# Optimization experiments

Measured on AMD Instinct MI355X. Metric: run time of the kernel, lower is better.

## Reference

```python
import jax, jax.numpy as jnp
import numpy as np
from functools import partial

IN_CH, OUT_CH, HID = 16, 20, 256
B, T = 64, 4096
LEAKY_SLOPE = 0.01  # torch LeakyReLU default


def _lstm_layer(x_seq, Wih, Whh, bih, bhh):
    """Single-layer LSTM over a full sequence.

    x_seq: (T, B, Din). Weights use PyTorch layout: W (4H, Din/H), gate order i,f,g,o.
    Returns hidden states (T, B, H).
    """
    H = Whh.shape[1]
    Tlen, Bsz = x_seq.shape[0], x_seq.shape[1]
    # Precompute input contributions for all timesteps in one GEMM.
    xw = jnp.einsum('tbd,gd->tbg', x_seq, Wih) + (bih + bhh)  # (T, B, 4H)

    def step(carry, xw_t):
        h, c = carry
        gates = xw_t + h @ Whh.T  # (B, 4H)
        i, f, g, o = jnp.split(gates, 4, axis=-1)
        i = jax.nn.sigmoid(i)
        f = jax.nn.sigmoid(f)
        g = jnp.tanh(g)
        o = jax.nn.sigmoid(o)
        c = f * c + i * g
        h = o * jnp.tanh(c)
        return (h, c), h

    h0 = jnp.zeros((Bsz, H), dtype=x_seq.dtype)
    c0 = jnp.zeros((Bsz, H), dtype=x_seq.dtype)
    _, hs = jax.lax.scan(step, (h0, c0), xw)
    return hs  # (T, B, H)


def setup_inputs() -> dict:
    key = jax.random.key(0)
    ks = jax.random.split(key, 12)
    s = 1.0 / np.sqrt(HID)  # torch nn.LSTM init scale
    return {
        'x': jax.random.normal(ks[0], (B, IN_CH, T), dtype=jnp.float32),
        'Wih0': jax.random.normal(ks[1], (4 * HID, IN_CH), dtype=jnp.float32) * s,
        'Whh0': jax.random.normal(ks[2], (4 * HID, HID), dtype=jnp.float32) * s,
        'bih0': jax.random.normal(ks[3], (4 * HID,), dtype=jnp.float32) * s,
        'bhh0': jax.random.normal(ks[4], (4 * HID,), dtype=jnp.float32) * s,
        'Wih1': jax.random.normal(ks[5], (4 * HID, HID), dtype=jnp.float32) * s,
        'Whh1': jax.random.normal(ks[6], (4 * HID, HID), dtype=jnp.float32) * s,
        'bih1': jax.random.normal(ks[7], (4 * HID,), dtype=jnp.float32) * s,
        'bhh1': jax.random.normal(ks[8], (4 * HID,), dtype=jnp.float32) * s,
        'Whead': jax.random.normal(ks[9], (OUT_CH, HID), dtype=jnp.float32) * s,
        'bhead': jax.random.normal(ks[10], (OUT_CH,), dtype=jnp.float32) * s,
    }


def reference(x, Wih0, Whh0, bih0, bhh0, Wih1, Whh1, bih1, bhh1, Whead, bhead):
    # x: (B, C_in, T) -> time-major (T, B, C_in)
    xs = jnp.transpose(x, (2, 0, 1))
    h1 = _lstm_layer(xs, Wih0, Whh0, bih0, bhh0)   # (T, B, H)
    h2 = _lstm_layer(h1, Wih1, Whh1, bih1, bhh1)   # (T, B, H)
    # Head: LeakyReLU then Linear, applied per timestep (vectorized).
    a = jnp.where(h2 >= 0, h2, LEAKY_SLOPE * h2)
    y = jnp.einsum('tbh,oh->tbo', a, Whead) + bhead  # (T, B, OUT)
    return jnp.transpose(y, (1, 2, 0))  # (B, C_out, T)
```

## Files before the change

### kernel.cpp

```cpp
#include <hip/hip_runtime.h>
#include <hip/hip_fp16.h>
#include <stdint.h>


#define T_SEQ 4096
#define NB    64
#define HID   256
#define G4    1024
#define INCH  16
#define OC    20

typedef _Float16 h2v   __attribute__((ext_vector_type(2)));
typedef _Float16 f16x8 __attribute__((ext_vector_type(8)));
typedef float    f32x4 __attribute__((ext_vector_type(4)));

__device__ __forceinline__ float fdot2(uint32_t a, uint32_t b, float c) {
  return __builtin_amdgcn_fdot2(__builtin_bit_cast(h2v, a),
                                __builtin_bit_cast(h2v, b), c, false);
}
__device__ __forceinline__ float sigf(float x) {
  x = fminf(fmaxf(x, -30.f), 30.f);
  return 1.f / (1.f + __expf(-x));
}
__device__ __forceinline__ float tanhf_fast(float x) {
  x = fminf(fmaxf(x, -15.f), 15.f);
  float e = __expf(-2.f * x);
  return (1.f - e) / (1.f + e);
}
__device__ __forceinline__ float quad_sum(float a) {
  a += __int_as_float(
      __builtin_amdgcn_update_dpp(0, __float_as_int(a), 0xB1, 0xF, 0xF, true));
  a += __int_as_float(
      __builtin_amdgcn_update_dpp(0, __float_as_int(a), 0x4E, 0xF, 0xF, true));
  return a;
}

#define PIN(x) asm volatile("" : "+v"(x))

struct SmemR {
  __half w[256 * 264];
  uint32_t hbuf[2][144];
  union {
    uint32_t xb[512 * 8];
    struct {
      __half abuf[2][320];
      __half whd[20 * 264];
      float  bh[20];
    } h1;
  } u;
};
struct SmemG {
  __half a[128 * 40];
  __half b[64 * 40];
};
union Smem { SmemR r; SmemG g; };

struct Params {
  const float* x;
  const __half *wh0, *wh1, *wi0, *wi1, *whd;
  const float  *bs0, *bs1, *bhd;
  float *h0s, *c0s, *h1s, *c1s;
  __half* h1w; const __half* h1r;
  float* xww;  const float* xwr;
  float* y;
  int L, Tc, nch;
};

template <int LAYER>
__device__ void role_rec(SmemR& S, int ch, const Params& P, int b) {
  if (ch < 0 || ch >= P.nch) return;
  const int tid   = threadIdx.x;
  const int slice = tid & 3;
  const int rg    = tid >> 2;
  const int Tc    = P.Tc;
  const __half* whh = (LAYER == 0) ? P.wh0 : P.wh1;

  for (int i = tid; i < 8192; i += 512) {
    int R = i >> 5, oct = i & 31;
    *(uint4*)&S.w[R * 264 + oct * 8] =
        *((const uint4*)(whh + (768 + R) * 256) + oct);
  }
  const int t0 = ch * Tc;
  if (LAYER == 0) {
    for (int i = tid; i < Tc * 8; i += 512) {
      int dp = i / Tc, tt = i - dp * Tc;
      float v0 = P.x[(b * INCH + 2 * dp) * T_SEQ + t0 + tt];
      float v1 = P.x[(b * INCH + 2 * dp + 1) * T_SEQ + t0 + tt];
      uint32_t pv = (uint32_t)__half_as_ushort(__float2half(v0)) |
                    ((uint32_t)__half_as_ushort(__float2half(v1)) << 16);
      S.u.xb[tt * 8 + dp] = pv;
    }
  } else {
    for (int i = tid; i < OC * 256; i += 512) {
      int o = i >> 8, k = i & 255;
      S.u.h1.whd[o * 264 + k] = P.whd[i];
    }
    if (tid < OC) S.u.h1.bh[tid] = P.bhd[tid];
  }

  uint32_t wr[6][32];
#pragma unroll
  for (int j = 0; j < 6; j++) {
    const uint4* p = (const uint4*)(whh + (rg + 128 * j) * 256 + slice * 64);
#pragma unroll
    for (int q = 0; q < 8; q++) {
      uint4 v = p[q];
      wr[j][4 * q] = v.x; wr[j][4 * q + 1] = v.y;
      wr[j][4 * q + 2] = v.z; wr[j][4 * q + 3] = v.w;
    }
  }
#pragma unroll
  for (int j = 0; j < 6; j++)
#pragma unroll
    for (int q = 0; q < 32; q++) PIN(wr[j][q]);

  uint32_t wx[8][2];
  if (LAYER == 0) {
#pragma unroll
    for (int j = 0; j < 8; j++) {
      const uint32_t* p = (const uint32_t*)(P.wi0 + (rg + 128 * j) * INCH + slice * 4);
      wx[j][0] = p[0]; wx[j][1] = p[1];
    }
#pragma unroll
    for (int j = 0; j < 8; j++) { PIN(wx[j][0]); PIN(wx[j][1]); }
  }

  const bool own = (slice < 2);
  const int chn = rg + ((slice & 1) << 7);
  float* hs = (LAYER == 0) ? P.h0s : P.h1s;
  float* cs = (LAYER == 0) ? P.c0s : P.c1s;
  float bs4[4] = {0.f, 0.f, 0.f, 0.f};
  float hO = 0.f, cO = 0.f;
  if (own) {
    const float* bsg = (LAYER == 0) ? P.bs0 : P.bs1;
#pragma unroll
    for (int k = 0; k < 4; k++) bs4[k] = bsg[chn + 256 * k];
    if (ch != 0) { hO = hs[b * 256 + chn]; cO = cs[b * 256 + chn]; }
    ((__half*)S.hbuf[0])[(chn >> 6) * 72 + (chn & 63)] = __float2half(hO);
  }
  const float* xp = (LAYER == 1 && own) ? (P.xwr + (size_t)b * G4 + chn)
                                        : (const float*)nullptr;
  __syncthreads();

  const __half* hbA = (const __half*)S.hbuf[0] + slice * 72;
  const __half* hbB = (const __half*)S.hbuf[1] + slice * 72;
  __half hprev = __float2half(0.f);
  float xwv[4] = {0.f, 0.f, 0.f, 0.f};

  for (int tt = 0; tt < Tc; ++tt) {
    if (LAYER == 0 && own && tt > 0)
      P.h1w[(size_t)((tt - 1) * NB + b) * 256 + chn] = hprev;
    if (LAYER == 1 && own) {
      const float* q = xp + (size_t)tt * (NB * G4);
      xwv[0] = q[0]; xwv[1] = q[256]; xwv[2] = q[512]; xwv[3] = q[768];
    }

    const __half* hb = (tt & 1) ? hbB : hbA;
    float acc[8];
#pragma unroll
    for (int j = 0; j < 8; j++) acc[j] = 0.f;

#pragma unroll
    for (int hf = 0; hf < 2; ++hf) {
      uint32_t hh[16];
      const uint4* hp = (const uint4*)(hb + hf * 32);
#pragma unroll
      for (int q = 0; q < 4; q++) {
        uint4 v = hp[q];
        hh[4 * q] = v.x; hh[4 * q + 1] = v.y; hh[4 * q + 2] = v.z; hh[4 * q + 3] = v.w;
      }
#pragma unroll
      for (int j = 0; j < 6; j++) {
        float a = acc[j];
#pragma unroll
        for (int q = 0; q < 16; q++) a = fdot2(wr[j][hf * 16 + q], hh[q], a);
        acc[j] = a;
      }
#pragma unroll
      for (int j = 6; j < 8; j++) {
        const uint4* wp =
            (const uint4*)&S.w[((j - 6) * 128 + rg) * 264 + slice * 64 + hf * 32];
        float a = acc[j];
#pragma unroll
        for (int q = 0; q < 4; q++) {
          uint4 v = wp[q];
          a = fdot2(v.x, hh[4 * q], a);
          a = fdot2(v.y, hh[4 * q + 1], a);
          a = fdot2(v.z, hh[4 * q + 2], a);
          a = fdot2(v.w, hh[4 * q + 3], a);
        }
        acc[j] = a;
      }
    }
    if (LAYER == 0) {
      uint32_t xv0 = S.u.xb[tt * 8 + 2 * slice];
      uint32_t xv1 = S.u.xb[tt * 8 + 2 * slice + 1];
#pragma unroll
      for (int j = 0; j < 8; j++) {
        acc[j] = fdot2(wx[j][0], xv0, acc[j]);
        acc[j] = fdot2(wx[j][1], xv1, acc[j]);
      }
    }
#pragma unroll
    for (int j = 0; j < 8; j++) acc[j] = quad_sum(acc[j]);

    if (own) {
      const int o = slice & 1;
      float gi = acc[0 + o] + bs4[0];
      float gf = acc[2 + o] + bs4[1];
      float gg = acc[4 + o] + bs4[2];
      float go = acc[6 + o] + bs4[3];
      if (LAYER == 1) { gi += xwv[0]; gf += xwv[1]; gg += xwv[2]; go += xwv[3]; }
      float iv = sigf(gi), fv = sigf(gf);
      float gv = tanhf_fast(gg), ov = sigf(go);
      cO = fv * cO + iv * gv;
      hO = ov * tanhf_fast(cO);
      __half h16 = __float2half(hO);
      ((__half*)S.hbuf[(tt + 1) & 1])[(chn >> 6) * 72 + (chn & 63)] = h16;
      if (LAYER == 0) {
        hprev = h16;
      } else {
        float av = hO > 0.f ? hO : 0.01f * hO;
        S.u.h1.abuf[tt & 1][(chn >> 5) * 40 + (chn & 31)] = __float2half(av);
      }
    }
    __syncthreads();

    if (LAYER == 1 && tid < OC * 8) {
      int o = tid >> 3, ks = tid & 7;
      const uint4* wp = (const uint4*)&S.u.h1.whd[o * 264 + ks * 32];
      const uint4* ap = (const uint4*)&S.u.h1.abuf[tt & 1][ks * 40];
      float a = 0.f;
#pragma unroll
      for (int q = 0; q < 4; q++) {
        uint4 w4 = wp[q];
        uint4 a4 = ap[q];
        a = fdot2(w4.x, a4.x, a);
        a = fdot2(w4.y, a4.y, a);
        a = fdot2(w4.z, a4.z, a);
        a = fdot2(w4.w, a4.w, a);
      }
      a += __shfl_xor(a, 1);
      a += __shfl_xor(a, 2);
      a += __shfl_xor(a, 4);
      if (ks == 0) P.y[(b * OC + o) * T_SEQ + t0 + tt] = a + S.u.h1.bh[o];
    }
  }
  if (own) {
    if (LAYER == 0)
      P.h1w[(size_t)((Tc - 1) * NB + b) * 256 + chn] = hprev;
    hs[b * 256 + chn] = hO;
    cs[b * 256 + chn] = cO;
  }
}

__device__ void role_gemm(SmemG& S, int chG, const Params& P) {
  if (chG < 0 || chG >= P.nch) return;
  const int bid = blockIdx.x - 128;
  const int nt = bid & 15, mt = bid >> 4;
  const int tb0 = mt * 128, g0 = nt * 64;
  const int tid = threadIdx.x, lane = tid & 63, w = tid >> 6;
  const int wm = w & 3, wn = w >> 2;

  f32x4 cacc[2][2] = {};
  for (int kk = 0; kk < 256; kk += 32) {
    __syncthreads();
    {
      int row = tid >> 2, q = tid & 3;
      const uint4* src = (const uint4*)(P.h1r + (tb0 + row) * 256 + kk + q * 8);
      *(uint4*)&S.a[row * 40 + q * 8] = *src;
    }
    if (tid < 256) {
      int row = tid >> 2, q = tid & 3;
      const uint4* src = (const uint4*)(P.wi1 + (g0 + row) * 256 + kk + q * 8);
      *(uint4*)&S.b[row * 40 + q * 8] = *src;
    }
    __syncthreads();
    f16x8 af[2], bf[2];
#pragma unroll
    for (int mi = 0; mi < 2; mi++)
      af[mi] = *(const f16x8*)&S.a[(wm * 32 + mi * 16 + (lane & 15)) * 40 + (lane >> 4) * 8];
#pragma unroll
    for (int ni = 0; ni < 2; ni++)
      bf[ni] = *(const f16x8*)&S.b[(wn * 32 + ni * 16 + (lane & 15)) * 40 + (lane >> 4) * 8];
#pragma unroll
    for (int mi = 0; mi < 2; mi++)
#pragma unroll
      for (int ni = 0; ni < 2; ni++)
        cacc[mi][ni] = __builtin_amdgcn_mfma_f32_16x16x32_f16(af[mi], bf[ni], cacc[mi][ni], 0, 0, 0);
  }
#pragma unroll
  for (int mi = 0; mi < 2; mi++)
#pragma unroll
    for (int ni = 0; ni < 2; ni++) {
      int m = wm * 32 + mi * 16 + (lane >> 4) * 4;
      int n = g0 + wn * 32 + ni * 16 + (lane & 15);
#pragma unroll
      for (int r = 0; r < 4; r++)
        P.xww[(size_t)(tb0 + m + r) * G4 + n] = cacc[mi][ni][r];
    }
}

__global__ __launch_bounds__(512)
__attribute__((amdgpu_waves_per_eu(2, 2)))
void fused_kernel(Params P) {
  __shared__ Smem S;
  int bid = blockIdx.x;
  if (bid < 64)        role_rec<0>(S.r, P.L, P, bid);
  else if (bid < 128)  role_rec<1>(S.r, P.L - 2, P, bid - 64);
  else                 role_gemm(S.g, P.L - 1, P);
}

__global__ void prep_kernel(const float* Wih0, const float* Whh0,
                            const float* bih0, const float* bhh0,
                            const float* Wih1, const float* Whh1,
                            const float* bih1, const float* bhh1,
                            const float* Whead, const float* bhead,
                            __half* wh0, __half* wh1, __half* wi1, __half* wi0,
                            __half* whd, float* bs0, float* bs1, float* bhd) {
  int i = blockIdx.x * blockDim.x + threadIdx.x;
  if (i < G4 * HID) {
    wh0[i] = __float2half(Whh0[i]);
    wh1[i] = __float2half(Whh1[i]);
    wi1[i] = __float2half(Wih1[i]);
  }
  if (i < G4 * INCH) wi0[i] = __float2half(Wih0[i]);
  if (i < OC * HID)  whd[i] = __float2half(Whead[i]);
  if (i < G4) { bs0[i] = bih0[i] + bhh0[i]; bs1[i] = bih1[i] + bhh1[i]; }
  if (i < OC) bhd[i] = bhead[i];
}

extern "C" void kernel_launch(void* const* d_in, const int* in_sizes, int n_in,
                              void* d_out, int out_size, void* d_ws, size_t ws_size,
                              hipStream_t stream) {
  const float* x     = (const float*)d_in[0];
  const float* Wih0  = (const float*)d_in[1];
  const float* Whh0  = (const float*)d_in[2];
  const float* bih0  = (const float*)d_in[3];
  const float* bhh0  = (const float*)d_in[4];
  const float* Wih1  = (const float*)d_in[5];
  const float* Whh1  = (const float*)d_in[6];
  const float* bih1  = (const float*)d_in[7];
  const float* bhh1  = (const float*)d_in[8];
  const float* Whead = (const float*)d_in[9];
  const float* bhead = (const float*)d_in[10];
  float* y = (float*)d_out;

  char* ws = (char*)d_ws;
  size_t cur = 0;
  auto alloc = [&](size_t sz) -> char* {
    char* p = ws + cur;
    cur = (cur + sz + 255) & ~(size_t)255;
    return p;
  };
  __half* wh0 = (__half*)alloc(G4 * HID * 2);
  __half* wh1 = (__half*)alloc(G4 * HID * 2);
  __half* wi1 = (__half*)alloc(G4 * HID * 2);
  __half* wi0 = (__half*)alloc(G4 * INCH * 2);
  __half* whd = (__half*)alloc(OC * HID * 2);
  float* bs0 = (float*)alloc(G4 * 4);
  float* bs1 = (float*)alloc(G4 * 4);
  float* bhd = (float*)alloc(OC * 4);
  float* h0s = (float*)alloc(NB * HID * 4);
  float* c0s = (float*)alloc(NB * HID * 4);
  float* h1s = (float*)alloc(NB * HID * 4);
  float* c1s = (float*)alloc(NB * HID * 4);
  size_t fixed = cur;

  int Tc = 512;
  while (Tc > 64) {
    size_t need = fixed + 2 * ((size_t)Tc * NB * HID * 2 + 512) +
                  2 * ((size_t)Tc * NB * G4 * 4 + 512);
    if (need <= ws_size) break;
    Tc >>= 1;
  }
  __half* h1buf[2];
  float* xwbuf[2];
  h1buf[0] = (__half*)alloc((size_t)Tc * NB * HID * 2);
  h1buf[1] = (__half*)alloc((size_t)Tc * NB * HID * 2);
  xwbuf[0] = (float*)alloc((size_t)Tc * NB * G4 * 4);
  xwbuf[1] = (float*)alloc((size_t)Tc * NB * G4 * 4);

  const int nch = T_SEQ / Tc;

  prep_kernel<<<(G4 * HID + 255) / 256, 256, 0, stream>>>(
      Wih0, Whh0, bih0, bhh0, Wih1, Whh1, bih1, bhh1, Whead, bhead,
      wh0, wh1, wi1, wi0, whd, bs0, bs1, bhd);

  const int ngemm = Tc * 8;
  for (int L = 0; L < nch + 2; ++L) {
    Params P;
    P.x = x;
    P.wh0 = wh0; P.wh1 = wh1; P.wi0 = wi0; P.wi1 = wi1; P.whd = whd;
    P.bs0 = bs0; P.bs1 = bs1; P.bhd = bhd;
    P.h0s = h0s; P.c0s = c0s; P.h1s = h1s; P.c1s = c1s;
    P.h1w = h1buf[L & 1];
    P.h1r = h1buf[(L + 1) & 1];
    P.xww = xwbuf[(L + 1) & 1];
    P.xwr = xwbuf[L & 1];
    P.y = y;
    P.L = L; P.Tc = Tc; P.nch = nch;
    fused_kernel<<<128 + ngemm, 512, 0, stream>>>(P);
  }
}
```

Measured before the change: 9.867 ms.

## Precompute layer-0 input projection one chunk ahead and store xw buffers in fp16

```diff
diff --git a/kernel.cpp b/kernel.cpp
--- a/kernel.cpp
+++ b/kernel.cpp
@@ -61,10 +61,54 @@
   const float  *bs0, *bs1, *bhd;
   float *h0s, *c0s, *h1s, *c1s;
   __half* h1w; const __half* h1r;
-  float* xww;  const float* xwr;
+  __half* xw1w; const __half* xw1r;
+  __half* xw0w; const __half* xw0r;
   float* y;
   int L, Tc, nch;
 };
+
+__device__ void compute_xw0(SmemR& S, int cc, const Params& P, int b,
+                            __half* out) {
+  const int tid = threadIdx.x;
+  const int Tc  = P.Tc;
+  const int t0  = cc * Tc;
+  for (int i = tid; i < Tc * 8; i += 512) {
+    int dp = i / Tc, tt = i - dp * Tc;
+    float v0 = P.x[(b * INCH + 2 * dp) * T_SEQ + t0 + tt];
+    float v1 = P.x[(b * INCH + 2 * dp + 1) * T_SEQ + t0 + tt];
+    uint32_t pv = (uint32_t)__half_as_ushort(__float2half(v0)) |
+                  ((uint32_t)__half_as_ushort(__float2half(v1)) << 16);
+    S.u.xb[tt * 8 + dp] = pv;
+  }
+  __syncthreads();
+  uint32_t w0[8], w1[8];
+  {
+    const uint4* p0 = (const uint4*)(P.wi0 + tid * INCH);
+    const uint4* p1 = (const uint4*)(P.wi0 + (tid + 512) * INCH);
+    uint4 a0 = p0[0], a1 = p0[1], b0 = p1[0], b1 = p1[1];
+    w0[0] = a0.x; w0[1] = a0.y; w0[2] = a0.z; w0[3] = a0.w;
+    w0[4] = a1.x; w0[5] = a1.y; w0[6] = a1.z; w0[7] = a1.w;
+    w1[0] = b0.x; w1[1] = b0.y; w1[2] = b0.z; w1[3] = b0.w;
+    w1[4] = b1.x; w1[5] = b1.y; w1[6] = b1.z; w1[7] = b1.w;
+  }
+  for (int tt = 0; tt < Tc; ++tt) {
+    uint32_t xv[8];
+    const uint4* xp = (const uint4*)&S.u.xb[tt * 8];
+    uint4 v0 = xp[0], v1 = xp[1];
+    xv[0] = v0.x; xv[1] = v0.y; xv[2] = v0.z; xv[3] = v0.w;
+    xv[4] = v1.x; xv[5] = v1.y; xv[6] = v1.z; xv[7] = v1.w;
+    float a0 = 0.f, a1 = 0.f;
+#pragma unroll
+    for (int q = 0; q < 8; ++q) {
+      a0 = fdot2(w0[q], xv[q], a0);
+      a1 = fdot2(w1[q], xv[q], a1);
+    }
+    __half* o = out + (size_t)(tt * NB + b) * G4;
+    o[tid]       = __float2half(a0);
+    o[tid + 512] = __float2half(a1);
+  }
+  __syncthreads();
+}
 
 template <int LAYER>
 __device__ void role_rec(SmemR& S, int ch, const Params& P, int b) {
@@ -82,14 +126,8 @@
   }
   const int t0 = ch * Tc;
   if (LAYER == 0) {
-    for (int i = tid; i < Tc * 8; i += 512) {
-      int dp = i / Tc, tt = i - dp * Tc;
-      float v0 = P.x[(b * INCH + 2 * dp) * T_SEQ + t0 + tt];
-      float v1 = P.x[(b * INCH + 2 * dp + 1) * T_SEQ + t0 + tt];
-      uint32_t pv = (uint32_t)__half_as_ushort(__float2half(v0)) |
-                    ((uint32_t)__half_as_ushort(__float2half(v1)) << 16);
-      S.u.xb[tt * 8 + dp] = pv;
-    }
+    if (ch == 0) compute_xw0(S, 0, P, b, P.xw0w == nullptr ? nullptr : (__half*)P.xw0r);
+    if (ch + 1 < P.nch) compute_xw0(S, ch + 1, P, b, P.xw0w);
   } else {
     for (int i = tid; i < OC * 256; i += 512) {
       int o = i >> 8, k = i & 255;
@@ -113,17 +151,6 @@
   for (int j = 0; j < 6; j++)
 #pragma unroll
     for (int q = 0; q < 32; q++) PIN(wr[j][q]);
-
-  uint32_t wx[8][2];
-  if (LAYER == 0) {
-#pragma unroll
-    for (int j = 0; j < 8; j++) {
-      const uint32_t* p = (const uint32_t*)(P.wi0 + (rg + 128 * j) * INCH + slice * 4);
-      wx[j][0] = p[0]; wx[j][1] = p[1];
-    }
-#pragma unroll
-    for (int j = 0; j < 8; j++) { PIN(wx[j][0]); PIN(wx[j][1]); }
-  }
 
   const bool own = (slice < 2);
   const int chn = rg + ((slice & 1) << 7);
@@ -138,67 +165,68 @@
     if (ch != 0) { hO = hs[b * 256 + chn]; cO = cs[b * 256 + chn]; }
     ((__half*)S.hbuf[0])[(chn >> 6) * 72 + (chn & 63)] = __float2half(hO);
   }
-  const float* xp = (LAYER == 1 && own) ? (P.xwr + (size_t)b * G4 + chn)
-                                        : (const float*)nullptr;
+  const __half* xp = nullptr;
+  if (own) xp = ((LAYER == 0) ? P.xw0r : P.xw1r) + (size_t)b * G4 + chn;
   __syncthreads();
 
   const __half* hbA = (const __half*)S.hbuf[0] + slice * 72;
   const __half* hbB = (const __half*)S.hbuf[1] + slice * 72;
+  const __half* wbase6 = &S.w[rg * 264 + slice * 64];
+  const __half* wbase7 = &S.w[(128 + rg) * 264 + slice * 64];
   __half hprev = __float2half(0.f);
-  float xwv[4] = {0.f, 0.f, 0.f, 0.f};
 
   for (int tt = 0; tt < Tc; ++tt) {
     if (LAYER == 0 && own && tt > 0)
       P.h1w[(size_t)((tt - 1) * NB + b) * 256 + chn] = hprev;
-    if (LAYER == 1 && own) {
-      const float* q = xp + (size_t)tt * (NB * G4);
-      xwv[0] = q[0]; xwv[1] = q[256]; xwv[2] = q[512]; xwv[3] = q[768];
+    float xwv[4] = {0.f, 0.f, 0.f, 0.f};
+    if (own) {
+      const __half* q = xp + (size_t)tt * (NB * G4);
+      xwv[0] = __half2float(q[0]);
+      xwv[1] = __half2float(q[256]);
+      xwv[2] = __half2float(q[512]);
+      xwv[3] = __half2float(q[768]);
     }
 
     const __half* hb = (tt & 1) ? hbB : hbA;
+    const uint4* hp = (const uint4*)hb;
     float acc[8];
 #pragma unroll
     for (int j = 0; j < 8; j++) acc[j] = 0.f;
 
 #pragma unroll
-    for (int hf = 0; hf < 2; ++hf) {
-      uint32_t hh[16];
-      const uint4* hp = (const uint4*)(hb + hf * 32);
-#pragma unroll
-      for (int q = 0; q < 4; q++) {
-        uint4 v = hp[q];
-        hh[4 * q] = v.x; hh[4 * q + 1] = v.y; hh[4 * q + 2] = v.z; hh[4 * q + 3] = v.w;
-      }
-#pragma unroll
-      for (int j = 0; j < 6; j++) {
+    for (int sb = 0; sb < 4; ++sb) {
+      uint32_t hh[8];
+      {
+        uint4 v0 = hp[2 * sb], v1 = hp[2 * sb + 1];
+        hh[0] = v0.x; hh[1] = v0.y; hh[2] = v0.z; hh[3] = v0.w;
+        hh[4] = v1.x; hh[5] = v1.y; hh[6] = v1.z; hh[7] = v1.w;
+      }
+#pragma unroll
+      for (int j = 0; j < 6; ++j) {
         float a = acc[j];
 #pragma unroll
-        for (int q = 0; q < 16; q++) a = fdot2(wr[j][hf * 16 + q], hh[q], a);
+        for (int q = 0; q < 8; ++q) a = fdot2(wr[j][8 * sb + q], hh[q], a);
         acc[j] = a;
       }
-#pragma unroll
-      for (int j = 6; j < 8; j++) {
-        const uint4* wp =
-            (const uint4*)&S.w[((j - 6) * 128 + rg) * 264 + slice * 64 + hf * 32];
-        float a = acc[j];
-#pragma unroll
-        for (int q = 0; q < 4; q++) {
-          uint4 v = wp[q];
-          a = fdot2(v.x, hh[4 * q], a);
-          a = fdot2(v.y, hh[4 * q + 1], a);
-          a = fdot2(v.z, hh[4 * q + 2], a);
-          a = fdot2(v.w, hh[4 * q + 3], a);
-        }
-        acc[j] = a;
-      }
-    }
-    if (LAYER == 0) {
-      uint32_t xv0 = S.u.xb[tt * 8 + 2 * slice];
-      uint32_t xv1 = S.u.xb[tt * 8 + 2 * slice + 1];
-#pragma unroll
-      for (int j = 0; j < 8; j++) {
-        acc[j] = fdot2(wx[j][0], xv0, acc[j]);
-        acc[j] = fdot2(wx[j][1], xv1, acc[j]);
+      {
+        const uint4* wp = (const uint4*)(wbase6 + sb * 16);
+        uint4 w0 = wp[0], w1 = wp[1];
+        float a = acc[6];
+        a = fdot2(w0.x, hh[0], a); a = fdot2(w0.y, hh[1], a);
+        a = fdot2(w0.z, hh[2], a); a = fdot2(w0.w, hh[3], a);
+        a = fdot2(w1.x, hh[4], a); a = fdot2(w1.y, hh[5], a);
+        a = fdot2(w1.z, hh[6], a); a = fdot2(w1.w, hh[7], a);
+        acc[6] = a;
+      }
+      {
+        const uint4* wp = (const uint4*)(wbase7 + sb * 16);
+        uint4 w0 = wp[0], w1 = wp[1];
+        float a = acc[7];
+        a = fdot2(w0.x, hh[0], a); a = fdot2(w0.y, hh[1], a);
+        a = fdot2(w0.z, hh[2], a); a = fdot2(w0.w, hh[3], a);
+        a = fdot2(w1.x, hh[4], a); a = fdot2(w1.y, hh[5], a);
+        a = fdot2(w1.z, hh[6], a); a = fdot2(w1.w, hh[7], a);
+        acc[7] = a;
       }
     }
 #pragma unroll
@@ -206,11 +234,10 @@
 
     if (own) {
       const int o = slice & 1;
-      float gi = acc[0 + o] + bs4[0];
-      float gf = acc[2 + o] + bs4[1];
-      float gg = acc[4 + o] + bs4[2];
-      float go = acc[6 + o] + bs4[3];
-      if (LAYER == 1) { gi += xwv[0]; gf += xwv[1]; gg += xwv[2]; go += xwv[3]; }
+      float gi = acc[0 + o] + bs4[0] + xwv[0];
+      float gf = acc[2 + o] + bs4[1] + xwv[1];
+      float gg = acc[4 + o] + bs4[2] + xwv[2];
+      float go = acc[6 + o] + bs4[3] + xwv[3];
       float iv = sigf(gi), fv = sigf(gf);
       float gv = tanhf_fast(gg), ov = sigf(go);
       cO = fv * cO + iv * gv;
@@ -297,7 +324,7 @@
       int n = g0 + wn * 32 + ni * 16 + (lane & 15);
 #pragma unroll
       for (int r = 0; r < 4; r++)
-        P.xww[(size_t)(tb0 + m + r) * G4 + n] = cacc[mi][ni][r];
+        P.xw1w[(size_t)(tb0 + m + r) * G4 + n] = __float2half(cacc[mi][ni][r]);
     }
 }
 
@@ -370,16 +397,19 @@
   int Tc = 512;
   while (Tc > 64) {
     size_t need = fixed + 2 * ((size_t)Tc * NB * HID * 2 + 512) +
-                  2 * ((size_t)Tc * NB * G4 * 4 + 512);
+                  4 * ((size_t)Tc * NB * G4 * 2 + 512);
     if (need <= ws_size) break;
     Tc >>= 1;
   }
   __half* h1buf[2];
-  float* xwbuf[2];
-  h1buf[0] = (__half*)alloc((size_t)Tc * NB * HID * 2);
-  h1buf[1] = (__half*)alloc((size_t)Tc * NB * HID * 2);
-  xwbuf[0] = (float*)alloc((size_t)Tc * NB * G4 * 4);
-  xwbuf[1] = (float*)alloc((size_t)Tc * NB * G4 * 4);
+  __half* xw1buf[2];
+  __half* xw0buf[2];
+  h1buf[0]  = (__half*)alloc((size_t)Tc * NB * HID * 2);
+  h1buf[1]  = (__half*)alloc((size_t)Tc * NB * HID * 2);
+  xw1buf[0] = (__half*)alloc((size_t)Tc * NB * G4 * 2);
+  xw1buf[1] = (__half*)alloc((size_t)Tc * NB * G4 * 2);
+  xw0buf[0] = (__half*)alloc((size_t)Tc * NB * G4 * 2);
+  xw0buf[1] = (__half*)alloc((size_t)Tc * NB * G4 * 2);
 
   const int nch = T_SEQ / Tc;
 
@@ -396,8 +426,10 @@
     P.h0s = h0s; P.c0s = c0s; P.h1s = h1s; P.c1s = c1s;
     P.h1w = h1buf[L & 1];
     P.h1r = h1buf[(L + 1) & 1];
-    P.xww = xwbuf[(L + 1) & 1];
-    P.xwr = xwbuf[L & 1];
+    P.xw1w = xw1buf[(L + 1) & 1];
+    P.xw1r = xw1buf[L & 1];
+    P.xw0w = xw0buf[(L + 1) & 1];
+    P.xw0r = xw0buf[L & 1];
     P.y = y;
     P.L = L; P.Tc = Tc; P.nch = nch;
     fused_kernel<<<128 + ngemm, 512, 0, stream>>>(P);
```

Measured after the change: 11.98 ms. 21.4% more time.
